# Optimization experiments

Hardware: AMD Instinct MI355X
Metric: run time of the kernel (lower is better)

The kernel has to match this reference:

```python
import jax, jax.numpy as jnp
import numpy as np

NEG_INF = -1e9  # stand-in for -INF in masked_fill

def setup_inputs() -> dict:
    key = jax.random.key(0)
    kq, kk, kv, km = jax.random.split(key, 4)
    B, H, S, D = 4, 16, 2048, 128
    query = jax.random.normal(kq, (B, H, S, D), dtype=jnp.float32)
    k_ = jax.random.normal(kk, (B, H, S, D), dtype=jnp.float32)
    value = jax.random.normal(kv, (B, H, S, D), dtype=jnp.float32)
    mask = jax.random.randint(km, (B, 1, 1, S), 0, 2, dtype=jnp.int32)
    return {"query": query, "key": k_, "value": value, "mask": mask}

def reference(query, key, value, mask):
    # _score: dot-product score  [B,H,Sq,Sk]
    score = jnp.einsum("bhqd,bhkd->bhqk", query, key)
    # _probability_normalize: masked_fill(mask==0, -INF) then softmax over keys
    score = jnp.where(mask == 0, NEG_INF, score)
    probability = jax.nn.softmax(score, axis=-1)
    # _attention_aggregate: probability @ value -> [B,H,Sq,D]
    return jnp.einsum("bhqk,bhkd->bhqd", probability, value)
```

## Files before the change

kernel.cpp:

```cpp
#include <hip/hip_runtime.h>

typedef _Float16 f16;
typedef _Float16 f16x8 __attribute__((ext_vector_type(8)));
typedef _Float16 f16x4 __attribute__((ext_vector_type(4)));
typedef float f32x4 __attribute__((ext_vector_type(4)));
typedef float f32x16 __attribute__((ext_vector_type(16)));
typedef unsigned short ushort_t;
typedef unsigned int uint_t;

#define SEQ 2048
#define DIM 128
#define KVBLK 64
#define NTMAX (SEQ / KVBLK)
#define TILE_BYTES 16384

typedef __attribute__((address_space(3))) char lds_char;
typedef __attribute__((address_space(1))) const char glb_char;

__device__ __forceinline__ void gload16(const void* g, void* l) {
  __builtin_amdgcn_global_load_lds((glb_char*)g, (lds_char*)l, 16, 0, 0);
}

__global__ __launch_bounds__(64)
void scan_mask(const int* __restrict__ Mg, int* __restrict__ cidx, int* __restrict__ ncomp) {
  const int b = blockIdx.x;
  const int l = threadIdx.x;
  int m[32];
  int cnt = 0;
  const int* mp = Mg + (size_t)b * SEQ + l * 32;
#pragma unroll
  for (int j = 0; j < 32; ++j) { m[j] = mp[j]; cnt += (m[j] != 0) ? 1 : 0; }
  int inc = cnt;
  for (int ofs = 1; ofs < 64; ofs <<= 1) {
    int v = __shfl_up(inc, ofs);
    if (l >= ofs) inc += v;
  }
  int pos = inc - cnt;
  int* cp = cidx + (size_t)b * SEQ;
  for (int j = 0; j < 32; ++j)
    if (m[j] != 0) cp[pos++] = l * 32 + j;
  if (l == 63) ncomp[b] = inc;
}

__global__ __launch_bounds__(256)
void prep_k(const float* __restrict__ Kg, char* __restrict__ Kws,
            const int* __restrict__ cidx, const int* __restrict__ ncomp) {
  const int tid  = threadIdx.x;
  const int blk  = blockIdx.x;
  const int head = blk >> 5, t = blk & 31;
  const int b    = head >> 4;
  const int nc   = ncomp[b];
  if (t >= ((nc + 63) >> 6)) return;
  const float* hin = Kg + (size_t)head * SEQ * DIM;
  const int* cp = cidx + (size_t)b * SEQ;
  char* out = Kws + (size_t)blk * TILE_BYTES;
#pragma unroll
  for (int i = 0; i < 4; ++i) {
    int u = i * 256 + tid;
    int krow = u >> 4;
    int un   = u & 15;
    int kidx = t * 64 + krow;
    union { f16 h[8]; uint4 u4; } c;
    if (kidx < nc) {
      const float* p = hin + (size_t)cp[kidx] * DIM + un * 8;
      float4 a = *(const float4*)p;
      float4 bq = *(const float4*)(p + 4);
      c.h[0]=(f16)a.x;  c.h[1]=(f16)a.y;  c.h[2]=(f16)a.z;  c.h[3]=(f16)a.w;
      c.h[4]=(f16)bq.x; c.h[5]=(f16)bq.y; c.h[6]=(f16)bq.z; c.h[7]=(f16)bq.w;
    } else {
      c.u4 = uint4{0, 0, 0, 0};
    }
    *(uint4*)(out + krow * 256 + ((un ^ (krow & 7)) << 4)) = c.u4;
  }
}

__global__ __launch_bounds__(256)
void prep_v(const float* __restrict__ Vg, char* __restrict__ Vws,
            const int* __restrict__ cidx, const int* __restrict__ ncomp) {
  __shared__ ushort_t Vs[KVBLK * 133];
  const int tid  = threadIdx.x;
  const int blk  = blockIdx.x;
  const int head = blk >> 5, t = blk & 31;
  const int b    = head >> 4;
  const int nc   = ncomp[b];
  if (t >= ((nc + 63) >> 6)) return;
  const float* hin = Vg + (size_t)head * SEQ * DIM;
  const int* cp = cidx + (size_t)b * SEQ;
  char* out = Vws + (size_t)blk * TILE_BYTES;
#pragma unroll
  for (int i = 0; i < 4; ++i) {
    int u = i * 256 + tid;
    int k  = u >> 4;
    int d0 = (u & 15) * 8;
    int kidx = t * 64 + k;
    f16 h[8];
    if (kidx < nc) {
      const float* p = hin + (size_t)cp[kidx] * DIM + d0;
      float4 a = *(const float4*)p;
      float4 bq = *(const float4*)(p + 4);
      h[0]=(f16)a.x;  h[1]=(f16)a.y;  h[2]=(f16)a.z;  h[3]=(f16)a.w;
      h[4]=(f16)bq.x; h[5]=(f16)bq.y; h[6]=(f16)bq.z; h[7]=(f16)bq.w;
    } else {
#pragma unroll
      for (int j = 0; j < 8; ++j) h[j] = (f16)0.f;
    }
#pragma unroll
    for (int j = 0; j < 8; ++j)
      Vs[k * 133 + d0 + j] = __builtin_bit_cast(ushort_t, h[j]);
  }
  __syncthreads();
#pragma unroll
  for (int i = 0; i < 4; ++i) {
    int u = i * 256 + tid;
    int d  = u >> 3;
    int un = u & 7;
    union { f16 h[8]; uint4 u4; } c;
#pragma unroll
    for (int j = 0; j < 8; ++j)
      c.h[j] = __builtin_bit_cast(f16, Vs[(un * 8 + j) * 133 + d]);
    *(uint4*)(out + d * 128 + ((un ^ (d & 7)) << 4)) = c.u4;
  }
}

__global__ __launch_bounds__(512, 2)
void attn_main32(const float* __restrict__ Qg, const char* __restrict__ Kws,
                 const char* __restrict__ Vws, const int* __restrict__ ncomp,
                 float* __restrict__ Og) {
  __shared__ __align__(16) char Kb[2][TILE_BYTES];
  __shared__ __align__(16) char Vb[2][TILE_BYTES];

  const int tid  = threadIdx.x;
  const int lane = tid & 63;
  const int w    = tid >> 6;
  const int q32  = lane & 31;
  const int h    = lane >> 5;

  const int bid  = blockIdx.x;
  const int head = (bid & 7) * 8 + (bid >> 6);
  const int qblk = (bid >> 3) & 7;
  const size_t hbase = (size_t)head * SEQ * DIM;
  const int bb = head >> 4;

  const int nc  = ncomp[bb];
  const int ntb = (nc + 63) >> 6;

  const char* ktb = Kws + ((size_t)(head * NTMAX) << 14);
  const char* vtb = Vws + ((size_t)(head * NTMAX) << 14);

  const int qrow = qblk * 256 + w * 32 + q32;

  f16x8 qf[8];
  {
    const float* qp = Qg + hbase + (size_t)qrow * DIM + h * 8;
#pragma unroll
    for (int c = 0; c < 8; ++c) {
      float4 a = *(const float4*)(qp + c * 16);
      float4 b = *(const float4*)(qp + c * 16 + 4);
      f16x8 f;
      f[0]=(f16)a.x; f[1]=(f16)a.y; f[2]=(f16)a.z; f[3]=(f16)a.w;
      f[4]=(f16)b.x; f[5]=(f16)b.y; f[6]=(f16)b.z; f[7]=(f16)b.w;
      qf[c] = f;
    }
  }

  f32x16 oacc[4];
#pragma unroll
  for (int dvt = 0; dvt < 4; ++dvt) oacc[dvt] = (f32x16)(0.f);
  float mrow = -INFINITY, lrow = 0.f;

  {
#pragma unroll
    for (int i = 0; i < 2; ++i) {
      int u = i * 512 + tid;
      gload16(ktb + u * 16, &Kb[0][u * 16]);
      gload16(vtb + u * 16, &Vb[0][u * 16]);
    }
  }
  __syncthreads();

  int cur = 0;
  for (int t = 0; t < ntb; ++t) {
    if (t + 1 < ntb) {
      const char* kt2 = ktb + ((size_t)(t + 1) << 14);
      const char* vt2 = vtb + ((size_t)(t + 1) << 14);
      const int nb = cur ^ 1;
#pragma unroll
      for (int i = 0; i < 2; ++i) {
        int u = i * 512 + tid;
        gload16(kt2 + u * 16, &Kb[nb][u * 16]);
        gload16(vt2 + u * 16, &Vb[nb][u * 16]);
      }
    }

    f32x16 s[2];
#pragma unroll
    for (int kt2 = 0; kt2 < 2; ++kt2) {
      const int kb = t * 64 + kt2 * 32;
      if (kb + 32 <= nc) {
        s[kt2] = (f32x16)(0.f);
      } else {
#pragma unroll
        for (int ri = 0; ri < 16; ++ri)
          s[kt2][ri] = (kb + (ri >> 2) * 8 + 4 * h + (ri & 3) < nc) ? 0.f : -1e9f;
      }
      const int krow = kt2 * 32 + q32;
      const int ksw  = krow & 7;
      __builtin_amdgcn_s_setprio(1);
#pragma unroll
      for (int c = 0; c < 8; ++c) {
        f16x8 kf = *(const f16x8*)(&Kb[cur][krow * 256 + (((2 * c + h) ^ ksw) << 4)]);
        s[kt2] = __builtin_amdgcn_mfma_f32_32x32x16_f16(kf, qf[c], s[kt2], 0, 0, 0);
      }
      __builtin_amdgcn_s_setprio(0);
    }

    float pmax = s[0][0];
#pragma unroll
    for (int r = 1; r < 16; ++r) pmax = fmaxf(pmax, s[0][r]);
#pragma unroll
    for (int r = 0; r < 16; ++r) pmax = fmaxf(pmax, s[1][r]);
    pmax = fmaxf(pmax, __shfl_xor(pmax, 32));

    if (!__all(pmax - mrow <= 8.f)) {
      float mnew = fmaxf(mrow, pmax);
      float scf = __expf(mrow - mnew);
#pragma unroll
      for (int dvt = 0; dvt < 4; ++dvt)
#pragma unroll
        for (int r = 0; r < 16; ++r) oacc[dvt][r] *= scf;
      lrow *= scf;
      mrow = mnew;
    }

    float psum = 0.f;
#pragma unroll
    for (int t2 = 0; t2 < 2; ++t2)
#pragma unroll
      for (int r = 0; r < 16; ++r) {
        float p = __expf(s[t2][r] - mrow);
        s[t2][r] = p;
        psum += p;
      }
    psum += __shfl_xor(psum, 32);
    lrow += psum;

    uint_t pkA[2][4], pkB[2][4];
#pragma unroll
    for (int t2 = 0; t2 < 2; ++t2)
#pragma unroll
      for (int m = 0; m < 4; ++m) {
        pkA[t2][m] = __builtin_bit_cast(uint_t,
            __builtin_amdgcn_cvt_pkrtz(s[t2][4 * m + 0], s[t2][4 * m + 1]));
        pkB[t2][m] = __builtin_bit_cast(uint_t,
            __builtin_amdgcn_cvt_pkrtz(s[t2][4 * m + 2], s[t2][4 * m + 3]));
      }

#pragma unroll
    for (int ks = 0; ks < 4; ++ks) {
      const int sk = ks & 1, tt = ks >> 1;
      uint_t Ao = h ? pkA[tt][2 * sk + 1] : pkA[tt][2 * sk];
      uint_t Bo = h ? pkB[tt][2 * sk + 1] : pkB[tt][2 * sk];
      uint_t As = h ? pkA[tt][2 * sk]     : pkA[tt][2 * sk + 1];
      uint_t Bs = h ? pkB[tt][2 * sk]     : pkB[tt][2 * sk + 1];
      uint_t Ax = (uint_t)__shfl_xor((int)As, 32);
      uint_t Bx = (uint_t)__shfl_xor((int)Bs, 32);
      union { uint_t u[4]; f16x8 v; } pa;
      pa.u[0] = h ? Ax : Ao;
      pa.u[1] = h ? Bx : Bo;
      pa.u[2] = h ? Ao : Ax;
      pa.u[3] = h ? Bo : Bx;
      __builtin_amdgcn_s_setprio(1);
#pragma unroll
      for (int dvt = 0; dvt < 4; ++dvt) {
        const int dv = dvt * 32 + q32;
        f16x8 vf = *(const f16x8*)(&Vb[cur][dv * 128 + (((2 * ks + h) ^ (dv & 7)) << 4)]);
        oacc[dvt] = __builtin_amdgcn_mfma_f32_32x32x16_f16(vf, pa.v, oacc[dvt], 0, 0, 0);
      }
      __builtin_amdgcn_s_setprio(0);
    }

    __syncthreads();
    cur ^= 1;
  }

  const float inv = 1.0f / lrow;
  float* op = Og + hbase + (size_t)qrow * DIM;
#pragma unroll
  for (int dvt = 0; dvt < 4; ++dvt)
#pragma unroll
    for (int rq = 0; rq < 4; ++rq) {
      float4 o4;
      o4.x = oacc[dvt][4 * rq + 0] * inv;
      o4.y = oacc[dvt][4 * rq + 1] * inv;
      o4.z = oacc[dvt][4 * rq + 2] * inv;
      o4.w = oacc[dvt][4 * rq + 3] * inv;
      *(float4*)(op + dvt * 32 + rq * 8 + h * 4) = o4;
    }
}

#define QT 64
#define P_STRIDE 72
#define VT_STRIDE 76
typedef _Float16 f16x4_t __attribute__((ext_vector_type(4)));
__global__ __launch_bounds__(256, 2)
void attn_fwd_fb(const float* __restrict__ Qg, const float* __restrict__ Kg,
                 const float* __restrict__ Vg, const int* __restrict__ Mg,
                 float* __restrict__ Og) {
  __shared__ __align__(16) ushort_t K_lds[QT * DIM];
  __shared__ __align__(16) ushort_t Vt_lds[DIM * VT_STRIDE];
  __shared__ __align__(16) ushort_t P_lds[QT * P_STRIDE];
  __shared__ int M_lds[KVBLK];
  const int tid  = threadIdx.x;
  const int lane = tid & 63;
  const int w    = tid >> 6;
  const int li   = lane & 15;
  const int g    = lane >> 4;
  const int bid  = blockIdx.x;
  const int nid  = (bid & 7) * 256 + (bid >> 3);
  const int head = nid >> 5;
  const int qblk = nid & 31;
  const size_t hbase = (size_t)head * SEQ * DIM;
  const int bb = head >> 4;
  f16x8 qf[4];
  {
    const float* qp = Qg + hbase + (size_t)(qblk * QT + w * 16 + li) * DIM + g * 8;
#pragma unroll
    for (int d0 = 0; d0 < 4; ++d0) {
      float4 a = *(const float4*)(qp + d0 * 32);
      float4 b = *(const float4*)(qp + d0 * 32 + 4);
      f16x8 f;
      f[0]=(f16)a.x; f[1]=(f16)a.y; f[2]=(f16)a.z; f[3]=(f16)a.w;
      f[4]=(f16)b.x; f[5]=(f16)b.y; f[6]=(f16)b.z; f[7]=(f16)b.w;
      qf[d0] = f;
    }
  }
  float mrow[4], lrow[4];
  f32x4 oacc[8];
#pragma unroll
  for (int r = 0; r < 4; ++r) { mrow[r] = -INFINITY; lrow[r] = 0.f; }
#pragma unroll
  for (int dt = 0; dt < 8; ++dt) oacc[dt] = (f32x4)(0.f);
  for (int t = 0; t < NTMAX; ++t) {
    const int k0 = t * KVBLK;
    __syncthreads();
    {
      const float4* kgp = (const float4*)(Kg + hbase + (size_t)k0 * DIM);
#pragma unroll
      for (int rr = 0; rr < 8; ++rr) {
        int fi = rr * 256 + tid;
        int krow = fi >> 5;
        int d4 = fi & 31;
        float4 v = kgp[fi];
        union { f16 h[4]; uint2 u; } c;
        c.h[0]=(f16)v.x; c.h[1]=(f16)v.y; c.h[2]=(f16)v.z; c.h[3]=(f16)v.w;
        int off = krow * 256 + ((d4 * 8) ^ ((krow & 7) << 4));
        *(uint2*)((char*)K_lds + off) = c.u;
      }
    }
    {
      const float* vgp = Vg + hbase + (size_t)k0 * DIM;
#pragma unroll
      for (int rr = 0; rr < 16; ++rr) {
        int u = rr * 256 + tid;
        int d = u & 127;
        int k2 = (u >> 7) * 2;
        float v0 = vgp[(size_t)k2 * DIM + d];
        float v1 = vgp[(size_t)(k2 + 1) * DIM + d];
        union { f16 h[2]; unsigned int u32; } c;
        c.h[0]=(f16)v0; c.h[1]=(f16)v1;
        *(unsigned int*)(Vt_lds + d * VT_STRIDE + k2) = c.u32;
      }
    }
    if (tid < KVBLK) M_lds[tid] = Mg[(size_t)bb * SEQ + k0 + tid];
    __syncthreads();
    f32x4 sacc[4];
#pragma unroll
    for (int kt = 0; kt < 4; ++kt) sacc[kt] = (f32x4)(0.f);
#pragma unroll
    for (int kt = 0; kt < 4; ++kt) {
      const int krow = kt * 16 + li;
      const int swz = (krow & 7) << 4;
#pragma unroll
      for (int d0 = 0; d0 < 4; ++d0) {
        f16x8 kf = *(const f16x8*)((const char*)K_lds + krow * 256 + ((d0 * 64 + g * 16) ^ swz));
        sacc[kt] = __builtin_amdgcn_mfma_f32_16x16x32_f16(qf[d0], kf, sacc[kt], 0, 0, 0);
      }
    }
    float tmax[4] = {-INFINITY, -INFINITY, -INFINITY, -INFINITY};
#pragma unroll
    for (int kt = 0; kt < 4; ++kt) {
      const bool ok = (M_lds[kt * 16 + li] != 0);
#pragma unroll
      for (int r = 0; r < 4; ++r) {
        float sv = ok ? sacc[kt][r] : -1e9f;
        sacc[kt][r] = sv;
        tmax[r] = fmaxf(tmax[r], sv);
      }
    }
#pragma unroll
    for (int r = 0; r < 4; ++r) {
      tmax[r] = fmaxf(tmax[r], __shfl_xor(tmax[r], 1));
      tmax[r] = fmaxf(tmax[r], __shfl_xor(tmax[r], 2));
      tmax[r] = fmaxf(tmax[r], __shfl_xor(tmax[r], 4));
      tmax[r] = fmaxf(tmax[r], __shfl_xor(tmax[r], 8));
    }
    float sc[4], psum[4];
#pragma unroll
    for (int r = 0; r < 4; ++r) {
      float mnew = fmaxf(mrow[r], tmax[r]);
      sc[r] = __expf(mrow[r] - mnew);
      mrow[r] = mnew;
      psum[r] = 0.f;
    }
#pragma unroll
    for (int dt = 0; dt < 8; ++dt)
#pragma unroll
      for (int r = 0; r < 4; ++r) oacc[dt][r] *= sc[r];
#pragma unroll
    for (int kt = 0; kt < 4; ++kt) {
#pragma unroll
      for (int r = 0; r < 4; ++r) {
        float p = __expf(sacc[kt][r] - mrow[r]);
        psum[r] += p;
        P_lds[(w * 16 + g * 4 + r) * P_STRIDE + kt * 16 + li] =
            __builtin_bit_cast(ushort_t, (f16)p);
      }
    }
#pragma unroll
    for (int r = 0; r < 4; ++r) {
      psum[r] += __shfl_xor(psum[r], 1);
      psum[r] += __shfl_xor(psum[r], 2);
      psum[r] += __shfl_xor(psum[r], 4);
      psum[r] += __shfl_xor(psum[r], 8);
      lrow[r] = lrow[r] * sc[r] + psum[r];
    }
#pragma unroll
    for (int c = 0; c < 2; ++c) {
      f16x8 pa = *(const f16x8*)(P_lds + (w * 16 + li) * P_STRIDE + c * 32 + g * 8);
#pragma unroll
      for (int dt = 0; dt < 8; ++dt) {
        const ushort_t* vp = Vt_lds + (dt * 16 + li) * VT_STRIDE + c * 32 + g * 8;
        f16x4_t v0 = *(const f16x4_t*)vp;
        f16x4_t v1 = *(const f16x4_t*)(vp + 4);
        f16x8 vf;
        vf[0]=v0[0]; vf[1]=v0[1]; vf[2]=v0[2]; vf[3]=v0[3];
        vf[4]=v1[0]; vf[5]=v1[1]; vf[6]=v1[2]; vf[7]=v1[3];
        oacc[dt] = __builtin_amdgcn_mfma_f32_16x16x32_f16(pa, vf, oacc[dt], 0, 0, 0);
      }
    }
  }
#pragma unroll
  for (int r = 0; r < 4; ++r) {
    float inv = 1.0f / lrow[r];
    float* op = Og + hbase + (size_t)(qblk * QT + w * 16 + g * 4 + r) * DIM + li;
#pragma unroll
    for (int dt = 0; dt < 8; ++dt) op[dt * 16] = oacc[dt][r] * inv;
  }
}

extern "C" void kernel_launch(void* const* d_in, const int* in_sizes, int n_in,
                              void* d_out, int out_size, void* d_ws, size_t ws_size,
                              hipStream_t stream) {
  (void)in_sizes; (void)n_in; (void)out_size;
  const float* Q = (const float*)d_in[0];
  const float* K = (const float*)d_in[1];
  const float* V = (const float*)d_in[2];
  const int*   M = (const int*)d_in[3];
  float*       O = (float*)d_out;

  const size_t half = (size_t)2048 * TILE_BYTES;
  const size_t cidx_off  = 2 * half;
  const size_t ncomp_off = cidx_off + (size_t)4 * SEQ * sizeof(int);
  const size_t need = ncomp_off + 4 * sizeof(int);

  if (ws_size >= need) {
    char* Kws = (char*)d_ws;
    char* Vws = Kws + half;
    int*  cidx  = (int*)((char*)d_ws + cidx_off);
    int*  ncomp = (int*)((char*)d_ws + ncomp_off);
    scan_mask<<<dim3(4), dim3(64), 0, stream>>>(M, cidx, ncomp);
    prep_k<<<dim3(2048), dim3(256), 0, stream>>>(K, Kws, cidx, ncomp);
    prep_v<<<dim3(2048), dim3(256), 0, stream>>>(V, Vws, cidx, ncomp);
    attn_main32<<<dim3(512), dim3(512), 0, stream>>>(Q, Kws, Vws, ncomp, O);
  } else {
    attn_fwd_fb<<<dim3(2048), dim3(256), 0, stream>>>(Q, K, V, M, O);
  }
}
```

Measured before the change: 143.9 us.

## Use partial vmcnt waits with raw barriers, widen K swizzle, tree-reduce softmax

Replaces __syncthreads with explicit s_waitcnt vmcnt(4) plus s_barrier, so the loop waits only for the current tile's async LDS loads while the next tile's prefetch stays in flight. It also widens the K-tile XOR swizzle from 8 to 16 chunks to cut LDS bank conflicts on K reads. The row max and exp-sum become tree reductions to shorten serial dependency chains. The manual vmcnt count depends on how many loads the compiler emits, and a wrong count would be a correctness risk.

```diff
diff --git a/kernel.cpp b/kernel.cpp
--- a/kernel.cpp
+++ b/kernel.cpp
@@ -70,7 +70,7 @@
     } else {
       c.u4 = uint4{0, 0, 0, 0};
     }
-    *(uint4*)(out + krow * 256 + ((un ^ (krow & 7)) << 4)) = c.u4;
+    *(uint4*)(out + krow * 256 + ((un ^ (krow & 15)) << 4)) = c.u4;
   }
 }
 
@@ -131,9 +131,10 @@
 
   const int tid  = threadIdx.x;
   const int lane = tid & 63;
-  const int w    = tid >> 6;
   const int q32  = lane & 31;
   const int h    = lane >> 5;
+  const int w    = tid >> 6;
+  (void)w;
 
   const int bid  = blockIdx.x;
   const int head = (bid & 7) * 8 + (bid >> 6);
@@ -147,7 +148,7 @@
   const char* ktb = Kws + ((size_t)(head * NTMAX) << 14);
   const char* vtb = Vws + ((size_t)(head * NTMAX) << 14);
 
-  const int qrow = qblk * 256 + w * 32 + q32;
+  const int qrow = qblk * 256 + (tid >> 6) * 32 + q32;
 
   f16x8 qf[8];
   {
@@ -168,15 +169,12 @@
   for (int dvt = 0; dvt < 4; ++dvt) oacc[dvt] = (f32x16)(0.f);
   float mrow = -INFINITY, lrow = 0.f;
 
-  {
-#pragma unroll
-    for (int i = 0; i < 2; ++i) {
-      int u = i * 512 + tid;
-      gload16(ktb + u * 16, &Kb[0][u * 16]);
-      gload16(vtb + u * 16, &Vb[0][u * 16]);
-    }
-  }
-  __syncthreads();
+#pragma unroll
+  for (int i = 0; i < 2; ++i) {
+    int u = i * 512 + tid;
+    gload16(ktb + u * 16, &Kb[0][u * 16]);
+    gload16(vtb + u * 16, &Vb[0][u * 16]);
+  }
 
   int cur = 0;
   for (int t = 0; t < ntb; ++t) {
@@ -190,7 +188,12 @@
         gload16(kt2 + u * 16, &Kb[nb][u * 16]);
         gload16(vt2 + u * 16, &Vb[nb][u * 16]);
       }
-    }
+      asm volatile("s_waitcnt vmcnt(4)" ::: "memory");
+    } else {
+      asm volatile("s_waitcnt vmcnt(0)" ::: "memory");
+    }
+    __builtin_amdgcn_s_barrier();
+    asm volatile("" ::: "memory");
 
     f32x16 s[2];
 #pragma unroll
@@ -204,7 +207,7 @@
           s[kt2][ri] = (kb + (ri >> 2) * 8 + 4 * h + (ri & 3) < nc) ? 0.f : -1e9f;
       }
       const int krow = kt2 * 32 + q32;
-      const int ksw  = krow & 7;
+      const int ksw  = krow & 15;
       __builtin_amdgcn_s_setprio(1);
 #pragma unroll
       for (int c = 0; c < 8; ++c) {
@@ -214,11 +217,14 @@
       __builtin_amdgcn_s_setprio(0);
     }
 
-    float pmax = s[0][0];
-#pragma unroll
-    for (int r = 1; r < 16; ++r) pmax = fmaxf(pmax, s[0][r]);
-#pragma unroll
-    for (int r = 0; r < 16; ++r) pmax = fmaxf(pmax, s[1][r]);
+    float mx[16];
+#pragma unroll
+    for (int r = 0; r < 16; ++r) mx[r] = fmaxf(s[0][r], s[1][r]);
+#pragma unroll
+    for (int r = 0; r < 8; ++r) mx[r] = fmaxf(mx[r], mx[r + 8]);
+#pragma unroll
+    for (int r = 0; r < 4; ++r) mx[r] = fmaxf(mx[r], mx[r + 4]);
+    float pmax = fmaxf(fmaxf(mx[0], mx[1]), fmaxf(mx[2], mx[3]));
     pmax = fmaxf(pmax, __shfl_xor(pmax, 32));
 
     if (!__all(pmax - mrow <= 8.f)) {
@@ -232,15 +238,18 @@
       mrow = mnew;
     }
 
-    float psum = 0.f;
-#pragma unroll
-    for (int t2 = 0; t2 < 2; ++t2)
-#pragma unroll
-      for (int r = 0; r < 16; ++r) {
-        float p = __expf(s[t2][r] - mrow);
-        s[t2][r] = p;
-        psum += p;
-      }
+    float ps[16];
+#pragma unroll
+    for (int r = 0; r < 16; ++r) {
+      s[0][r] = __expf(s[0][r] - mrow);
+      s[1][r] = __expf(s[1][r] - mrow);
+      ps[r] = s[0][r] + s[1][r];
+    }
+#pragma unroll
+    for (int r = 0; r < 8; ++r) ps[r] += ps[r + 8];
+#pragma unroll
+    for (int r = 0; r < 4; ++r) ps[r] += ps[r + 4];
+    float psum = (ps[0] + ps[1]) + (ps[2] + ps[3]);
     psum += __shfl_xor(psum, 32);
     lrow += psum;
 
@@ -279,7 +288,9 @@
       __builtin_amdgcn_s_setprio(0);
     }
 
-    __syncthreads();
+    asm volatile("" ::: "memory");
+    __builtin_amdgcn_s_barrier();
+    asm volatile("" ::: "memory");
     cur ^= 1;
   }
 
```

After: 143.6 us. Within noise of the previous version (-0.2%).
